# Performance work log

Measured on AMD Instinct MI355X. Metric: run time of the kernel, lower is better.

Reference implementation:

```python
import jax, jax.numpy as jnp
import numpy as np

B, K, C = 32, 512, 32  # batch, node count (spatial size), hardcoded out channels


def setup_inputs() -> dict:
    key = jax.random.key(0)
    k1, k2, k3, k4, k5 = jax.random.split(key, 5)
    x = jax.random.normal(k1, (B, 1, K, K), dtype=jnp.float32)
    # torch Conv2d default init: U(-1/sqrt(fan_in), 1/sqrt(fan_in)), fan_in = 1*K
    s = 1.0 / np.sqrt(K).astype(np.float32)
    w_col = jax.random.uniform(k2, (C, K), jnp.float32, -s, s)  # Conv2d(1,32,(1,K)) weight
    b_col = jax.random.uniform(k3, (C,), jnp.float32, -s, s)
    w_row = jax.random.uniform(k4, (C, K), jnp.float32, -s, s)  # Conv2d(1,32,(K,1)) weight
    b_row = jax.random.uniform(k5, (C,), jnp.float32, -s, s)
    return {"input": x, "w_col": w_col, "b_col": b_col, "w_row": w_row, "b_row": b_row}


def reference(input, w_col, b_col, w_row, b_row):
    x = input[:, 0]  # [B,K,K]
    # conv_column: kernel (1,K) -> per-row dot with w_col -> [B,C,K] (spatial [K,1] squeezed)
    col = jnp.einsum('bik,ok->boi', x, w_col) + b_col[None, :, None]
    # conv_row: kernel (K,1) -> per-column dot with w_row -> [B,C,K] (spatial [1,K] squeezed)
    row = jnp.einsum('bkj,ok->boj', x, w_row) + b_row[None, :, None]
    # cat([conv_row]*K, dim=2) makes every row equal to `row`; cat([conv_column]*K, dim=3)
    # makes every column equal to `col`. Their matmul is the constant dot(row, col)
    # broadcast over the whole KxK output (exactly the original math, reduced).
    s = jnp.einsum('bok,bok->bo', row, col)  # [B,C]
    Bn, Cn = s.shape
    return jnp.broadcast_to(s[:, :, None, None], (Bn, Cn, x.shape[1], x.shape[2]))
```

## Files before the change

### kernel.cpp

```cpp
#include <hip/hip_runtime.h>

#define Bn 32
#define Kn 512
#define Cn 32

typedef float vf4 __attribute__((ext_vector_type(4)));

#define WTC_OFF   0
#define WTR_OFF   16384
#define COL_OFF   32768
#define ROW_OFF   557056
#define S_OFF     1081344

__global__ void k_transpose_w(const float* __restrict__ w_col,
                              const float* __restrict__ w_row,
                              float* __restrict__ ws) {
    int idx = blockIdx.x * blockDim.x + threadIdx.x;
    int which = idx >> 14;
    int e = idx & 16383;
    int o = e & 31, k = e >> 5;
    const float* src = which ? w_row : w_col;
    float* dst = ws + (which ? WTR_OFF : WTC_OFF);
    dst[e] = src[o * Kn + k];
}

__global__ __launch_bounds__(256) void k_colrow(
    const float* __restrict__ x,
    const float* __restrict__ bcol,
    const float* __restrict__ brow,
    float* __restrict__ ws) {
    const int chunk = blockIdx.x;
    const int b     = blockIdx.y;
    const int phase = blockIdx.z;
    const int t0  = chunk * 128;
    const int tid = threadIdx.x;
    const int t   = tid & 127;
    const int kh  = tid >> 7;

    __shared__ float s_x[64 * 129];

    const float* __restrict__ wT = ws + (phase ? WTR_OFF : WTC_OFF);
    const float* __restrict__ xb = x + b * (Kn * Kn);

    float acc[32];
#pragma unroll
    for (int o = 0; o < 32; ++o) acc[o] = 0.f;

    if (phase == 0) {
        const float4* x4 = (const float4*)xb;
        for (int tile = 0; tile < 8; ++tile) {
            __syncthreads();
#pragma unroll
            for (int i = 0; i < 8; ++i) {
                int idx4 = tid + i * 256;
                int tl = idx4 >> 4;
                int k4 = idx4 & 15;
                float4 v = x4[(t0 + tl) * 128 + tile * 16 + k4];
                s_x[(k4 * 4 + 0) * 129 + tl] = v.x;
                s_x[(k4 * 4 + 1) * 129 + tl] = v.y;
                s_x[(k4 * 4 + 2) * 129 + tl] = v.z;
                s_x[(k4 * 4 + 3) * 129 + tl] = v.w;
            }
            __syncthreads();
            const int kkb = kh * 32;
            const float* __restrict__ wTt = wT + (tile * 64 + kkb) * 32;
#pragma unroll 4
            for (int kk = 0; kk < 32; ++kk) {
                float xv = s_x[(kkb + kk) * 129 + t];
                const float* __restrict__ w = wTt + kk * 32;
#pragma unroll
                for (int o = 0; o < 32; ++o) acc[o] = fmaf(xv, w[o], acc[o]);
            }
        }
    } else {
        const int kb = kh * 256;
#pragma unroll 4
        for (int k = 0; k < 256; ++k) {
            float xv = xb[(kb + k) * Kn + t0 + t];
            const float* __restrict__ w = wT + (kb + k) * 32;
#pragma unroll
            for (int o = 0; o < 32; ++o) acc[o] = fmaf(xv, w[o], acc[o]);
        }
    }

    float* red = s_x;
    __syncthreads();
    if (kh == 1) {
#pragma unroll
        for (int o = 0; o < 32; ++o) red[t * 33 + o] = acc[o];
    }
    __syncthreads();
    if (kh == 0) {
        const float* __restrict__ bias = phase ? brow : bcol;
        float* __restrict__ dst = ws + (phase ? ROW_OFF : COL_OFF) + (b * Kn + t0 + t) * 32;
#pragma unroll
        for (int o = 0; o < 32; ++o)
            dst[o] = acc[o] + red[t * 33 + o] + bias[o];
    }
}

__global__ void k_reduce(float* __restrict__ ws) {
    const int b = blockIdx.x;
    const int tid = threadIdx.x;
    const int o = tid & 31, tp = tid >> 5;
    const float* __restrict__ cp = ws + COL_OFF + b * (Kn * 32);
    const float* __restrict__ rp = ws + ROW_OFF + b * (Kn * 32);
    float sum = 0.f;
    for (int j = 0; j < 64; ++j) {
        int tt = tp * 64 + j;
        sum += cp[tt * 32 + o] * rp[tt * 32 + o];
    }
    __shared__ float red[8 * 33];
    red[tp * 33 + o] = sum;
    __syncthreads();
    if (tid < 32) {
        float s = 0.f;
#pragma unroll
        for (int j = 0; j < 8; ++j) s += red[j * 33 + tid];
        ws[S_OFF + b * 32 + tid] = s;
    }
}

__global__ __launch_bounds__(256) void k_broadcast(const float* __restrict__ ws,
                                                   float* __restrict__ out) {
    const int bo   = blockIdx.x >> 4;
    const int part = blockIdx.x & 15;
    const float sval = ws[S_OFF + bo];
    vf4 v = (vf4){sval, sval, sval, sval};
    vf4* __restrict__ out4 =
        (vf4*)out + (size_t)bo * 65536 + (size_t)part * 4096 + threadIdx.x;
#pragma unroll
    for (int j = 0; j < 16; ++j)
        __builtin_nontemporal_store(v, out4 + j * 256);
}

extern "C" void kernel_launch(void* const* d_in, const int* in_sizes, int n_in,
                              void* d_out, int out_size, void* d_ws, size_t ws_size,
                              hipStream_t stream) {
    const float* x     = (const float*)d_in[0];
    const float* w_col = (const float*)d_in[1];
    const float* b_col = (const float*)d_in[2];
    const float* w_row = (const float*)d_in[3];
    const float* b_row = (const float*)d_in[4];
    float* out = (float*)d_out;
    float* ws  = (float*)d_ws;

    hipLaunchKernelGGL(k_transpose_w, dim3(128), dim3(256), 0, stream, w_col, w_row, ws);
    hipLaunchKernelGGL(k_colrow, dim3(4, 32, 2), dim3(256), 0, stream, x, b_col, b_row, ws);
    hipLaunchKernelGGL(k_reduce, dim3(32), dim3(256), 0, stream, ws);
    hipLaunchKernelGGL(k_broadcast, dim3(16384), dim3(256), 0, stream, ws, out);
}
```

Baseline: 1.184 ms.

## Split K-reduction four ways in colrow and parallelize final reduce with atomics

The col/row projection kernel now gives each block 64 output positions with four thread groups splitting the K reduction, instead of 128 positions with two groups. This doubles the grid to 512 blocks for better CU occupancy, at the cost of a two-stage shared-memory reduction. The per-batch dot-product reduce is spread over four blocks per batch that combine through atomicAdd into a buffer the prep kernel now zeroes. The result is still dominated by the broadcast write of the 128 MB output.

```diff
diff --git a/kernel.cpp b/kernel.cpp
--- a/kernel.cpp
+++ b/kernel.cpp
@@ -12,10 +12,14 @@
 #define ROW_OFF   557056
 #define S_OFF     1081344
 
-__global__ void k_transpose_w(const float* __restrict__ w_col,
-                              const float* __restrict__ w_row,
-                              float* __restrict__ ws) {
-    int idx = blockIdx.x * blockDim.x + threadIdx.x;
+__global__ void k_prep(const float* __restrict__ w_col,
+                       const float* __restrict__ w_row,
+                       float* __restrict__ ws) {
+    if (blockIdx.x == 128) {
+        ((vf4*)(ws + S_OFF))[threadIdx.x] = (vf4){0.f, 0.f, 0.f, 0.f};
+        return;
+    }
+    int idx = blockIdx.x * 256 + threadIdx.x;
     int which = idx >> 14;
     int e = idx & 16383;
     int o = e & 31, k = e >> 5;
@@ -32,12 +36,13 @@
     const int chunk = blockIdx.x;
     const int b     = blockIdx.y;
     const int phase = blockIdx.z;
-    const int t0  = chunk * 128;
+    const int t0  = chunk * 64;
     const int tid = threadIdx.x;
-    const int t   = tid & 127;
-    const int kh  = tid >> 7;
+    const int t   = tid & 63;
+    const int kh  = tid >> 6;
 
-    __shared__ float s_x[64 * 129];
+    __shared__ float s_x[64 * 65];
+    __shared__ float red[2][64 * 33];
 
     const float* __restrict__ wT = ws + (phase ? WTR_OFF : WTC_OFF);
     const float* __restrict__ xb = x + b * (Kn * Kn);
@@ -51,31 +56,30 @@
         for (int tile = 0; tile < 8; ++tile) {
             __syncthreads();
 #pragma unroll
-            for (int i = 0; i < 8; ++i) {
+            for (int i = 0; i < 4; ++i) {
                 int idx4 = tid + i * 256;
                 int tl = idx4 >> 4;
                 int k4 = idx4 & 15;
                 float4 v = x4[(t0 + tl) * 128 + tile * 16 + k4];
-                s_x[(k4 * 4 + 0) * 129 + tl] = v.x;
-                s_x[(k4 * 4 + 1) * 129 + tl] = v.y;
-                s_x[(k4 * 4 + 2) * 129 + tl] = v.z;
-                s_x[(k4 * 4 + 3) * 129 + tl] = v.w;
+                s_x[(k4 * 4 + 0) * 65 + tl] = v.x;
+                s_x[(k4 * 4 + 1) * 65 + tl] = v.y;
+                s_x[(k4 * 4 + 2) * 65 + tl] = v.z;
+                s_x[(k4 * 4 + 3) * 65 + tl] = v.w;
             }
             __syncthreads();
-            const int kkb = kh * 32;
-            const float* __restrict__ wTt = wT + (tile * 64 + kkb) * 32;
-#pragma unroll 4
-            for (int kk = 0; kk < 32; ++kk) {
-                float xv = s_x[(kkb + kk) * 129 + t];
+            const float* __restrict__ wTt = wT + (tile * 64 + kh * 16) * 32;
+#pragma unroll
+            for (int kk = 0; kk < 16; ++kk) {
+                float xv = s_x[(kh * 16 + kk) * 65 + t];
                 const float* __restrict__ w = wTt + kk * 32;
 #pragma unroll
                 for (int o = 0; o < 32; ++o) acc[o] = fmaf(xv, w[o], acc[o]);
             }
         }
     } else {
-        const int kb = kh * 256;
-#pragma unroll 4
-        for (int k = 0; k < 256; ++k) {
+        const int kb = kh * 128;
+#pragma unroll 8
+        for (int k = 0; k < 128; ++k) {
             float xv = xb[(kb + k) * Kn + t0 + t];
             const float* __restrict__ w = wT + (kb + k) * 32;
 #pragma unroll
@@ -83,11 +87,22 @@
         }
     }
 
-    float* red = s_x;
+    __syncthreads();
+    if (kh >= 2) {
+        float* r = red[kh - 2];
+#pragma unroll
+        for (int o = 0; o < 32; ++o) r[t * 33 + o] = acc[o];
+    }
+    __syncthreads();
+    if (kh < 2) {
+        const float* r = red[kh];
+#pragma unroll
+        for (int o = 0; o < 32; ++o) acc[o] += r[t * 33 + o];
+    }
     __syncthreads();
     if (kh == 1) {
 #pragma unroll
-        for (int o = 0; o < 32; ++o) red[t * 33 + o] = acc[o];
+        for (int o = 0; o < 32; ++o) red[1][t * 33 + o] = acc[o];
     }
     __syncthreads();
     if (kh == 0) {
@@ -95,19 +110,21 @@
         float* __restrict__ dst = ws + (phase ? ROW_OFF : COL_OFF) + (b * Kn + t0 + t) * 32;
 #pragma unroll
         for (int o = 0; o < 32; ++o)
-            dst[o] = acc[o] + red[t * 33 + o] + bias[o];
+            dst[o] = acc[o] + red[1][t * 33 + o] + bias[o];
     }
 }
 
 __global__ void k_reduce(float* __restrict__ ws) {
-    const int b = blockIdx.x;
+    const int tg = blockIdx.x & 3, b = blockIdx.x >> 2;
     const int tid = threadIdx.x;
     const int o = tid & 31, tp = tid >> 5;
     const float* __restrict__ cp = ws + COL_OFF + b * (Kn * 32);
     const float* __restrict__ rp = ws + ROW_OFF + b * (Kn * 32);
+    const int tbase = tg * 128 + tp * 16;
     float sum = 0.f;
-    for (int j = 0; j < 64; ++j) {
-        int tt = tp * 64 + j;
+#pragma unroll
+    for (int j = 0; j < 16; ++j) {
+        int tt = tbase + j;
         sum += cp[tt * 32 + o] * rp[tt * 32 + o];
     }
     __shared__ float red[8 * 33];
@@ -117,7 +134,7 @@
         float s = 0.f;
 #pragma unroll
         for (int j = 0; j < 8; ++j) s += red[j * 33 + tid];
-        ws[S_OFF + b * 32 + tid] = s;
+        atomicAdd(ws + S_OFF + b * 32 + tid, s);
     }
 }
 
@@ -145,8 +162,8 @@
     float* out = (float*)d_out;
     float* ws  = (float*)d_ws;
 
-    hipLaunchKernelGGL(k_transpose_w, dim3(128), dim3(256), 0, stream, w_col, w_row, ws);
-    hipLaunchKernelGGL(k_colrow, dim3(4, 32, 2), dim3(256), 0, stream, x, b_col, b_row, ws);
-    hipLaunchKernelGGL(k_reduce, dim3(32), dim3(256), 0, stream, ws);
+    hipLaunchKernelGGL(k_prep, dim3(129), dim3(256), 0, stream, w_col, w_row, ws);
+    hipLaunchKernelGGL(k_colrow, dim3(8, 32, 2), dim3(256), 0, stream, x, b_col, b_row, ws);
+    hipLaunchKernelGGL(k_reduce, dim3(128), dim3(256), 0, stream, ws);
     hipLaunchKernelGGL(k_broadcast, dim3(16384), dim3(256), 0, stream, ws, out);
 }
```

Result: faster. 1.146 ms (-3.2%).
